# Optimization experiments

Measured on AMD Instinct MI355X. Metric: run time of the kernel, lower is better.

## Reference

```python
import jax, jax.numpy as jnp
import numpy as np

P, C, D = 65536, 64, 256

def setup_inputs() -> dict:
    key = jax.random.key(0)
    k1, k2, k3, k4 = jax.random.split(key, 4)
    return {
        "protos1": jax.random.normal(k1, (P, D), dtype=jnp.float32),
        "protos2": jax.random.normal(k2, (P, D), dtype=jnp.float32),
        "W": jax.random.normal(k3, (D, D), dtype=jnp.float32) / np.float32(np.sqrt(D)),
        "b": jax.random.normal(k4, (D,), dtype=jnp.float32),
        "num_classes": C,
    }

def _pairwise_dist(x, y):
    # x: (C, n, D), y: (C, m, D) -> squared-euclidean-style dists (C, n, m)
    xs = jnp.sum(x * x, axis=-1)[:, :, None]
    ys = jnp.sum(y * y, axis=-1)[:, None, :]
    return xs + ys - 2.0 * jnp.einsum('cid,cjd->cij', x, y)

def reference(protos1, protos2, W, b, num_classes):
    nc = int(num_classes)
    d = protos1.shape[-1]
    # prototypes[c::num_classes] for all c at once: (P,D) -> (P//C, C, D) -> (C, P//C, D)
    p1 = protos1.reshape(-1, nc, d).transpose(1, 0, 2)
    p2 = protos2.reshape(-1, nc, d).transpose(1, 0, 2)
    # transition: nn.Linear -> x @ W.T + b ; inverse: (x - b) @ inv(W.T)
    p2_inv = (p2 - b) @ jnp.linalg.inv(W.T)
    p1_fwd = p1 @ W.T + b
    a = _pairwise_dist(p1, p2_inv)          # (C, n, n)
    bb = _pairwise_dist(p2, p1_fwd)         # (C, n, n)
    proto_losses_source = jnp.mean(jnp.min(a, axis=2), axis=1)   # (C,)
    proto_losses_target = jnp.mean(jnp.min(bb, axis=2), axis=1)  # (C,)
    return jnp.stack([proto_losses_source, proto_losses_target])  # (2, C)
```

## Files before the change

### kernel.cpp

```cpp
#include <hip/hip_runtime.h>

#define D 256
#define NC 64

using u16 = unsigned short;
using u32 = unsigned int;

typedef __attribute__((ext_vector_type(8))) short bfv8;
typedef __attribute__((ext_vector_type(4))) float f32x4;
typedef __attribute__((ext_vector_type(2))) int v2i;

__device__ __forceinline__ float bf2f(u32 u) {
  union { u32 i; float f; } v; v.i = u << 16; return v.f;
}
__device__ __forceinline__ u16 f2bf(float f) {
  union { float f; u32 i; } v; v.f = f;
  u32 x = v.i;
  return (u16)((x + 0x7FFFu + ((x >> 16) & 1u)) >> 16);
}
__device__ __forceinline__ u32 pk2(float a, float b) {
  return (u32)f2bf(a) | ((u32)f2bf(b) << 16);
}
__device__ __forceinline__ size_t cmrow(int g) {
  return (size_t)(((g & 63) << 10) | (g >> 6));
}

__device__ __forceinline__ void gload_lds16(const void* src, void* dst) {
  __builtin_amdgcn_global_load_lds(
      (const __attribute__((address_space(1))) void*)src,
      (__attribute__((address_space(3))) void*)dst, 16, 0, 0);
}

#define K1_LDS 74240
#define DISTP_LDS 70144

__device__ void gj_body(const float* __restrict__ W, float* __restrict__ IW,
                        char* smem) {
  float (*Ml)[20]    = (float(*)[20])smem;
  float (*Arow)[256] = (float(*)[256])(smem + 20480);
  float (*G)[256]    = (float(*)[256])(smem + 36864);
  u16*  Gfrag        = (u16*)(smem + 53248);
  float (*Pinv)[20]  = (float(*)[20])(smem + 69888);
  const int t = threadIdx.x, w = t >> 6, l = t & 63;
  const int lj = l & 15, lh = l >> 4;
  const int r0 = 16 * w;
  const bool lo32 = (l < 32);

  f32x4 x[16];
#pragma unroll
  for (int ct = 0; ct < 16; ++ct)
#pragma unroll
    for (int reg = 0; reg < 4; ++reg)
      x[ct][reg] = W[(size_t)(r0 + 4 * lh + reg) * D + 16 * ct + lj];

  for (int s = 0; s < 16; ++s) {
#pragma unroll
    for (int ct = 0; ct < 16; ++ct)
      if (ct == s)
#pragma unroll
        for (int reg = 0; reg < 4; ++reg)
          Ml[r0 + 4 * lh + reg][lj] = x[ct][reg];
    if (w == s) {
#pragma unroll
      for (int ct = 0; ct < 16; ++ct)
#pragma unroll
        for (int reg = 0; reg < 4; ++reg)
          Arow[4 * lh + reg][16 * ct + lj] = x[ct][reg];
    }
    bfv8 afr;
    {
      const int row = r0 + lj;
      float4 f0 = *(const float4*)&Ml[row][8 * (lh & 1)];
      float4 f1 = *(const float4*)&Ml[row][8 * (lh & 1) + 4];
      const float fv[8] = {f0.x, f0.y, f0.z, f0.w, f1.x, f1.y, f1.z, f1.w};
      union { bfv8 v; u16 e[8]; } A;
      if (lh < 2) {
#pragma unroll
        for (int e = 0; e < 8; ++e) A.e[e] = f2bf(-fv[e]);
      } else {
#pragma unroll
        for (int e = 0; e < 8; ++e) {
          const float hi = bf2f(f2bf(fv[e]));
          A.e[e] = f2bf(-(fv[e] - hi));
        }
      }
      afr = A.v;
    }
    __syncthreads();
    if (t < 16) {
      float p[16];
      {
        float4 rr0 = *(const float4*)&Ml[16 * s + t][0];
        float4 rr1 = *(const float4*)&Ml[16 * s + t][4];
        float4 rr2 = *(const float4*)&Ml[16 * s + t][8];
        float4 rr3 = *(const float4*)&Ml[16 * s + t][12];
        p[0] = rr0.x; p[1] = rr0.y; p[2] = rr0.z; p[3] = rr0.w;
        p[4] = rr1.x; p[5] = rr1.y; p[6] = rr1.z; p[7] = rr1.w;
        p[8] = rr2.x; p[9] = rr2.y; p[10] = rr2.z; p[11] = rr2.w;
        p[12] = rr3.x; p[13] = rr3.y; p[14] = rr3.z; p[15] = rr3.w;
      }
#pragma unroll
      for (int pp = 0; pp < 16; ++pp) {
        float u[16];
#pragma unroll
        for (int j = 0; j < 16; ++j)
          u[j] = __int_as_float(__builtin_amdgcn_readlane(__float_as_int(p[j]), pp));
        const float pv = u[pp];
        const float d = 1.0f / pv;
        if (t == pp) {
#pragma unroll
          for (int j = 0; j < 16; ++j) p[j] = u[j] * d;
          p[pp] = d;
        } else {
          const float md = p[pp] * d;
          u[pp] = pv + 1.0f;
#pragma unroll
          for (int j = 0; j < 16; ++j) p[j] = fmaf(-md, u[j], p[j]);
        }
      }
#pragma unroll
      for (int j = 0; j < 16; ++j) Pinv[t][j] = p[j];
    }
    __syncthreads();
    {
      const bool inC = ((l >> 2) == s);
      const int co = (l & 3) << 2;
      const int gct = l >> 2;
      const int kk = w;
      float4 g = make_float4(0.f, 0.f, 0.f, 0.f);
#pragma unroll
      for (int q = 0; q < 16; ++q) {
        const float pv = Pinv[kk][q];
        const float4 av = *(const float4*)&Arow[q][4 * l];
        g.x = fmaf(pv, av.x, g.x); g.y = fmaf(pv, av.y, g.y);
        g.z = fmaf(pv, av.z, g.z); g.w = fmaf(pv, av.w, g.w);
      }
      if (inC) {
        g.x = Pinv[kk][co + 0] + (kk == co + 0 ? 1.f : 0.f);
        g.y = Pinv[kk][co + 1] + (kk == co + 1 ? 1.f : 0.f);
        g.z = Pinv[kk][co + 2] + (kk == co + 2 ? 1.f : 0.f);
        g.w = Pinv[kk][co + 3] + (kk == co + 3 ? 1.f : 0.f);
      }
      *(float4*)&G[kk][4 * l] = g;
      const int e0 = kk & 7;
      const int lbase = 16 * (kk >> 3);
      const float gv[4] = {g.x, g.y, g.z, g.w};
#pragma unroll
      for (int cc = 0; cc < 4; ++cc) {
        const int cl = 4 * (l & 3) + cc;
        const u16 hi = f2bf(gv[cc]);
        const u16 lo = f2bf(gv[cc] - bf2f(hi));
        Gfrag[gct * 520 + (lbase + cl) * 8 + e0] = hi;
        Gfrag[gct * 520 + (32 + lbase + cl) * 8 + e0] = lo;
      }
    }
    __syncthreads();
    if (w != s) {
#pragma unroll
      for (int ct = 0; ct < 16; ++ct) {
        union { bfv8 v; uint4 u; } B1, B2;
        B1.v = *(const bfv8*)&Gfrag[ct * 520 + l * 8];
#if __has_builtin(__builtin_amdgcn_permlane32_swap)
        {
          v2i r;
          r = __builtin_amdgcn_permlane32_swap((int)B1.u.x, (int)B1.u.x, false, false);
          B2.u.x = lo32 ? (u32)r.y : (u32)r.x;
          r = __builtin_amdgcn_permlane32_swap((int)B1.u.y, (int)B1.u.y, false, false);
          B2.u.y = lo32 ? (u32)r.y : (u32)r.x;
          r = __builtin_amdgcn_permlane32_swap((int)B1.u.z, (int)B1.u.z, false, false);
          B2.u.z = lo32 ? (u32)r.y : (u32)r.x;
          r = __builtin_amdgcn_permlane32_swap((int)B1.u.w, (int)B1.u.w, false, false);
          B2.u.w = lo32 ? (u32)r.y : (u32)r.x;
        }
#else
        B2.v = *(const bfv8*)&Gfrag[ct * 520 + (l ^ 32) * 8];
#endif
        x[ct] = __builtin_amdgcn_mfma_f32_16x16x32_bf16(afr, B1.v, x[ct], 0, 0, 0);
        x[ct] = __builtin_amdgcn_mfma_f32_16x16x32_bf16(afr, B2.v, x[ct], 0, 0, 0);
      }
    } else {
#pragma unroll
      for (int ct = 0; ct < 16; ++ct) {
        if (ct == s) {
#pragma unroll
          for (int reg = 0; reg < 4; ++reg)
            x[ct][reg] = Pinv[4 * lh + reg][lj];
        } else {
#pragma unroll
          for (int reg = 0; reg < 4; ++reg)
            x[ct][reg] = G[4 * lh + reg][16 * ct + lj];
        }
      }
    }
    __syncthreads();
  }
#pragma unroll
  for (int ct = 0; ct < 16; ++ct)
#pragma unroll
    for (int reg = 0; reg < 4; ++reg)
      IW[(size_t)(r0 + 4 * lh + reg) * D + 16 * ct + lj] = x[ct][reg];
}

__device__ void convnorm_role(const float* __restrict__ P, u16* __restrict__ Pb,
                              float* __restrict__ nrm, int blk) {
  const int tx = threadIdx.x;
  const int r = tx >> 2, q = tx & 3;
  const int g = blk * 256 + r;
  const float* src = P + (size_t)g * D + q * 64;
  u16* dst = Pb + cmrow(g) * D + q * 64;
  float ss = 0.f;
#pragma unroll
  for (int g4 = 0; g4 < 8; ++g4) {
    float4 v0 = *(const float4*)(src + g4 * 8);
    float4 v1 = *(const float4*)(src + g4 * 8 + 4);
    ss = fmaf(v0.x, v0.x, fmaf(v0.y, v0.y, fmaf(v0.z, v0.z, fmaf(v0.w, v0.w, ss))));
    ss = fmaf(v1.x, v1.x, fmaf(v1.y, v1.y, fmaf(v1.z, v1.z, fmaf(v1.w, v1.w, ss))));
    uint4 w4;
    w4.x = pk2(v0.x, v0.y); w4.y = pk2(v0.z, v0.w);
    w4.z = pk2(v1.x, v1.y); w4.w = pk2(v1.z, v1.w);
    *(uint4*)(dst + g4 * 8) = w4;
  }
  ss += __shfl_xor(ss, 1, 64);
  ss += __shfl_xor(ss, 2, 64);
  if (q == 0) nrm[cmrow(g)] = ss;
}

template <int MODE>
__device__ void distp_body(const float* __restrict__ Pj,
                           const float* __restrict__ Wf,
                           const u16* __restrict__ BrowsBF,
                           const float* __restrict__ biasv,
                           const float* __restrict__ PanF,
                           const u16* __restrict__ PanBF,
                           const float* __restrict__ nB,
                           float* __restrict__ pmind, int bid, char* smem) {
  const int lb = (bid & 7) * 64 + (bid >> 3);
  const int c = lb >> 3, jt = lb & 7;
  const int tx = threadIdx.x, ww = tx >> 6, l = tx & 63;
  const int mw = ww >> 3, nw = ww & 7, l4 = l >> 4, lm = l & 15;
  char* Ab = smem;
  float* nfpart = (float*)(smem + 65536);
  float* minbuf = (float*)(smem + 65536);
  float* nAb = (float*)(smem + 69632);
  float* nbpart = (float*)(smem + 70144);

  auto issue_chunk = [&](int buf, int ch) {
#pragma unroll
    for (int u = 0; u < 2; ++u) {
      const int chunk = ww * 2 + u, ks = chunk >> 2, n = chunk & 3;
      const u16* src = PanBF + ((size_t)(c << 10) + ch * 64 + n * 16 + lm) * D
                       + ks * 32 + l4 * 8;
      gload_lds16(src, Ab + buf * 32768 + chunk * 1024);
    }
  };
  auto stage_f32 = [&](int buf, int ch) {
#pragma unroll
    for (int u = 0; u < 2; ++u) {
      const int chunk = ww * 2 + u, ks = chunk >> 2, n = chunk & 3;
      const int m = ch * 64 + n * 16 + lm;
      const float* src = PanF + ((size_t)m * 64 + c) * D + ks * 32 + l4 * 8;
      float4 v0 = *(const float4*)src;
      float4 v1 = *(const float4*)(src + 4);
      uint4 w4;
      w4.x = pk2(v0.x, v0.y); w4.y = pk2(v0.z, v0.w);
      w4.z = pk2(v1.x, v1.y); w4.w = pk2(v1.z, v1.w);
      *(uint4*)(Ab + buf * 32768 + chunk * 1024 + l * 16) = w4;
      float ss = fmaf(v0.x, v0.x, fmaf(v0.y, v0.y, fmaf(v0.z, v0.z, v0.w * v0.w)));
      ss = fmaf(v1.x, v1.x, fmaf(v1.y, v1.y, fmaf(v1.z, v1.z, fmaf(v1.w, v1.w, ss))));
      ss += __shfl_xor(ss, 16, 64);
      ss += __shfl_xor(ss, 32, 64);
      if (l4 == 0) nbpart[buf * 512 + ks * 64 + n * 16 + lm] = ss;
    }
  };

  bfv8 bfr[2][8];
  if (MODE == 0) {
#pragma unroll
    for (int nf2 = 0; nf2 < 2; ++nf2)
#pragma unroll
      for (int ks = 0; ks < 8; ++ks) {
        const float* wsrc = Wf + (size_t)(nw * 32 + nf2 * 16 + lm) * D + ks * 32 + l4 * 8;
        float4 b0 = *(const float4*)wsrc;
        float4 b1 = *(const float4*)(wsrc + 4);
        union { bfv8 v; uint4 u; } cv;
        cv.u.x = pk2(b0.x, b0.y); cv.u.y = pk2(b0.z, b0.w);
        cv.u.z = pk2(b1.x, b1.y); cv.u.w = pk2(b1.z, b1.w);
        bfr[nf2][ks] = cv.v;
      }
  } else {
#pragma unroll
    for (int nf2 = 0; nf2 < 2; ++nf2)
#pragma unroll
      for (int ks = 0; ks < 8; ++ks)
        bfr[nf2][ks] = *(const bfv8*)(BrowsBF +
            (size_t)(nw * 32 + nf2 * 16 + lm) * D + ks * 32 + l4 * 8);
  }
  {
    const int r = tx >> 3, sg = tx & 7;
    const float* arow = Pj + ((size_t)(jt * 128 + r) * NC + c) * D + sg * 32;
#pragma unroll
    for (int g2 = 0; g2 < 4; ++g2) {
      float4 v0 = *(const float4*)(arow + g2 * 8);
      float4 v1 = *(const float4*)(arow + g2 * 8 + 4);
      uint4 w4;
      w4.x = pk2(v0.x, v0.y); w4.y = pk2(v0.z, v0.w);
      w4.z = pk2(v1.x, v1.y); w4.w = pk2(v1.z, v1.w);
      *(uint4*)(Ab + (sg * 8 + (r >> 4)) * 1024 + ((r & 15) + g2 * 16) * 16) = w4;
    }
  }
  __syncthreads();
  const bfv8* A8 = (const bfv8*)Ab;
  f32x4 acc[4][2];
#pragma unroll
  for (int mf = 0; mf < 4; ++mf) {
    acc[mf][0] = f32x4{0.f, 0.f, 0.f, 0.f};
    acc[mf][1] = f32x4{0.f, 0.f, 0.f, 0.f};
  }
#pragma unroll
  for (int ks = 0; ks < 8; ++ks)
#pragma unroll
    for (int mf = 0; mf < 4; ++mf) {
      bfv8 a = A8[(ks * 8 + mw * 4 + mf) * 64 + l];
      acc[mf][0] = __builtin_amdgcn_mfma_f32_16x16x32_bf16(a, bfr[0][ks], acc[mf][0], 0, 0, 0);
      acc[mf][1] = __builtin_amdgcn_mfma_f32_16x16x32_bf16(a, bfr[1][ks], acc[mf][1], 0, 0, 0);
    }
  float bias[2];
  if (MODE == 0) {
#pragma unroll
    for (int nf2 = 0; nf2 < 2; ++nf2)
      bias[nf2] = biasv[nw * 32 + nf2 * 16 + lm];
  } else {
#pragma unroll
    for (int nf2 = 0; nf2 < 2; ++nf2) {
      float pd = 0.f;
#pragma unroll
      for (int ks = 0; ks < 8; ++ks) {
        float4 b0 = *(const float4*)(biasv + ks * 32 + l4 * 8);
        float4 b1 = *(const float4*)(biasv + ks * 32 + l4 * 8 + 4);
        pd = fmaf(b0.x, bf2f((u16)bfr[nf2][ks][0]), pd);
        pd = fmaf(b0.y, bf2f((u16)bfr[nf2][ks][1]), pd);
        pd = fmaf(b0.z, bf2f((u16)bfr[nf2][ks][2]), pd);
        pd = fmaf(b0.w, bf2f((u16)bfr[nf2][ks][3]), pd);
        pd = fmaf(b1.x, bf2f((u16)bfr[nf2][ks][4]), pd);
        pd = fmaf(b1.y, bf2f((u16)bfr[nf2][ks][5]), pd);
        pd = fmaf(b1.z, bf2f((u16)bfr[nf2][ks][6]), pd);
        pd = fmaf(b1.w, bf2f((u16)bfr[nf2][ks][7]), pd);
      }
      pd += __shfl_xor(pd, 16, 64);
      pd += __shfl_xor(pd, 32, 64);
      bias[nf2] = -pd;
    }
  }
  __syncthreads();
  u16* tile = (u16*)Ab;
#pragma unroll
  for (int mf = 0; mf < 4; ++mf)
#pragma unroll
    for (int rr = 0; rr < 4; ++rr) {
      const int j = mw * 64 + mf * 16 + l4 * 4 + rr;
      float v2 = 0.f;
#pragma unroll
      for (int nf2 = 0; nf2 < 2; ++nf2) {
        const float v = acc[mf][nf2][rr] + bias[nf2];
        const u16 hv = f2bf(v);
        tile[(((nw * 8 + mw * 4 + mf) << 6) + ((nf2 * 2 + (lm >> 3)) << 4)
              + l4 * 4 + rr) * 8 + (lm & 7)] = hv;
        const float vr = bf2f(hv);
        v2 = fmaf(vr, vr, v2);
      }
      v2 += __shfl_xor(v2, 1, 64);
      v2 += __shfl_xor(v2, 2, 64);
      v2 += __shfl_xor(v2, 4, 64);
      v2 += __shfl_xor(v2, 8, 64);
      if (lm == 0) nfpart[nw * 128 + j] = v2;
    }
  __syncthreads();
  const int jw = ww >> 2, iw = ww & 3;
  bfv8 afr[2][8];
#pragma unroll
  for (int jj = 0; jj < 2; ++jj)
#pragma unroll
    for (int ks = 0; ks < 8; ++ks)
      afr[jj][ks] = A8[(ks * 8 + jw * 2 + jj) * 64 + l];
  __syncthreads();
  if (MODE == 0) stage_f32(0, 0); else issue_chunk(0, 0);
  if (tx < 128) {
    float s = 0.f;
#pragma unroll
    for (int q = 0; q < 8; ++q) s += nfpart[q * 128 + tx];
    nAb[tx] = s;
  }
  __syncthreads();
  float naj[2][4];
#pragma unroll
  for (int jj = 0; jj < 2; ++jj)
#pragma unroll
    for (int rr = 0; rr < 4; ++rr)
      naj[jj][rr] = nAb[jw * 32 + jj * 16 + l4 * 4 + rr];
  const float* nBc = (MODE == 1) ? nB + (c << 10) : nullptr;
  const size_t obase = (size_t)(c * 8 + jt) * 1024;
  for (int ch = 0; ch < 16; ++ch) {
    if (ch < 15) {
      if (MODE == 0) stage_f32((ch + 1) & 1, ch + 1);
      else issue_chunk((ch + 1) & 1, ch + 1);
    }
    const bfv8* B8 = (const bfv8*)(Ab + (ch & 1) * 32768);
    f32x4 a2[2];
    a2[0] = f32x4{0.f, 0.f, 0.f, 0.f};
    a2[1] = f32x4{0.f, 0.f, 0.f, 0.f};
#pragma unroll
    for (int ks = 0; ks < 8; ++ks) {
      bfv8 b = B8[(ks * 4 + iw) * 64 + l];
      a2[0] = __builtin_amdgcn_mfma_f32_16x16x32_bf16(afr[0][ks], b, a2[0], 0, 0, 0);
      a2[1] = __builtin_amdgcn_mfma_f32_16x16x32_bf16(afr[1][ks], b, a2[1], 0, 0, 0);
    }
    float nb;
    if (MODE == 0) {
      const float* nbp = nbpart + (ch & 1) * 512;
      nb = nbp[iw * 16 + lm];
#pragma unroll
      for (int ks = 1; ks < 8; ++ks) nb += nbp[ks * 64 + iw * 16 + lm];
    } else {
      nb = nBc[ch * 64 + iw * 16 + lm];
    }
    float mm = 3.0e38f;
#pragma unroll
    for (int jj = 0; jj < 2; ++jj)
#pragma unroll
      for (int rr = 0; rr < 4; ++rr) {
        const float dd = nb + naj[jj][rr] - 2.0f * a2[jj][rr];
        mm = fminf(mm, dd);
      }
    mm = fminf(mm, __shfl_xor(mm, 16, 64));
    mm = fminf(mm, __shfl_xor(mm, 32, 64));
    if (l4 == 0) minbuf[jw * 64 + iw * 16 + lm] = mm;
    __syncthreads();
    if (tx < 64) {
      float m = minbuf[tx];
#pragma unroll
      for (int q = 1; q < 4; ++q) m = fminf(m, minbuf[q * 64 + tx]);
      pmind[obase + ch * 64 + tx] = m;
    }
    __syncthreads();
  }
}

__global__ __launch_bounds__(1024, 1) void k1_kernel(
    const float* __restrict__ p1, const float* __restrict__ p2,
    const float* __restrict__ W, const float* __restrict__ bv,
    float* __restrict__ pmin1, float* __restrict__ IWa,
    u16* __restrict__ p1b, float* __restrict__ n1) {
  extern __shared__ char smem[];
  const int b = blockIdx.x;
  if (b == 0) {
    gj_body(W, IWa, smem);
  } else if (b <= 512) {
    distp_body<0>(p1, W, nullptr, bv, p2, nullptr, nullptr, pmin1, b - 1, smem);
  } else {
    convnorm_role(p1, p1b, n1, b - 513);
  }
}

__global__ __launch_bounds__(256) void ns_fused(const float* __restrict__ W,
                                                const float* __restrict__ X,
                                                u16* __restrict__ Yb) {
  __shared__ float Xc[256][8];
  __shared__ float Rc[256][8];
  const int jc = blockIdx.x * 8, t = threadIdx.x;
  {
    float4 xa = *(const float4*)&X[(size_t)t * D + jc];
    float4 xb = *(const float4*)&X[(size_t)t * D + jc + 4];
    Xc[t][0] = xa.x; Xc[t][1] = xa.y; Xc[t][2] = xa.z; Xc[t][3] = xa.w;
    Xc[t][4] = xb.x; Xc[t][5] = xb.y; Xc[t][6] = xb.z; Xc[t][7] = xb.w;
  }
  __syncthreads();
  float r[8] = {0.f, 0.f, 0.f, 0.f, 0.f, 0.f, 0.f, 0.f};
#pragma unroll 4
  for (int k = 0; k < D; ++k) {
    const float wv = W[(size_t)t * D + k];
#pragma unroll
    for (int q = 0; q < 8; ++q) r[q] = fmaf(wv, Xc[k][q], r[q]);
  }
#pragma unroll
  for (int q = 0; q < 8; ++q)
    Rc[t][q] = ((t - jc) == q ? 2.0f : 0.0f) - r[q];
  __syncthreads();
  float y[8] = {0.f, 0.f, 0.f, 0.f, 0.f, 0.f, 0.f, 0.f};
#pragma unroll 4
  for (int k = 0; k < D; ++k) {
    const float xv = X[(size_t)t * D + k];
#pragma unroll
    for (int q = 0; q < 8; ++q) y[q] = fmaf(xv, Rc[k][q], y[q]);
  }
#pragma unroll
  for (int q = 0; q < 8; ++q)
    Yb[(size_t)t * D + jc + q] = f2bf(y[q]);
}

__global__ __launch_bounds__(1024, 1) void k3_kernel(
    const float* __restrict__ p2, const u16* __restrict__ IWb,
    const float* __restrict__ bv, const u16* __restrict__ p1b,
    const float* __restrict__ n1, float* __restrict__ pmin0) {
  extern __shared__ char smem[];
  distp_body<1>(p2, nullptr, IWb, bv, nullptr, p1b, n1, pmin0, blockIdx.x, smem);
}

__global__ __launch_bounds__(256) void final_kernel(const float* __restrict__ pmin,
                                                    float* __restrict__ out) {
  __shared__ float ws4[4];
  const int dc = blockIdx.x, tx = threadIdx.x;
  const float* base = pmin + (size_t)dc * 8192;
  float s = 0.f;
#pragma unroll
  for (int t = 0; t < 4; ++t) {
    const int i = t * 256 + tx;
    float m = base[i];
#pragma unroll
    for (int j = 1; j < 8; ++j) m = fminf(m, base[j * 1024 + i]);
    s += m;
  }
#pragma unroll
  for (int off = 32; off; off >>= 1) s += __shfl_xor(s, off, 64);
  if ((tx & 63) == 0) ws4[tx >> 6] = s;
  __syncthreads();
  if (tx == 0)
    out[dc] = (ws4[0] + ws4[1] + ws4[2] + ws4[3]) * (1.0f / 1024.0f);
}

extern "C" void kernel_launch(void* const* d_in, const int* in_sizes, int n_in,
                              void* d_out, int out_size, void* d_ws, size_t ws_size,
                              hipStream_t stream) {
  const float* p1 = (const float*)d_in[0];
  const float* p2 = (const float*)d_in[1];
  const float* W  = (const float*)d_in[2];
  const float* bv = (const float*)d_in[3];
  float* out = (float*)d_out;
  char* ws = (char*)d_ws;
  float* n1  = (float*)(ws);
  float* IWa = (float*)(ws + (256 << 10));
  u16* IWb   = (u16*)(ws + (512 << 10));
  float* pmin = (float*)(ws + (1 << 20));
  u16* p1b   = (u16*)(ws + (6u << 20));
  float* pmin0 = pmin;
  float* pmin1 = pmin + 524288;

  hipFuncSetAttribute((const void*)k1_kernel,
                      hipFuncAttributeMaxDynamicSharedMemorySize, K1_LDS);
  hipFuncSetAttribute((const void*)k3_kernel,
                      hipFuncAttributeMaxDynamicSharedMemorySize, DISTP_LDS);

  k1_kernel<<<769, 1024, K1_LDS, stream>>>(p1, p2, W, bv, pmin1, IWa, p1b, n1);
  ns_fused<<<32, 256, 0, stream>>>(W, IWa, IWb);
  k3_kernel<<<512, 1024, DISTP_LDS, stream>>>(p2, IWb, bv, p1b, n1, pmin0);
  final_kernel<<<128, 256, 0, stream>>>(pmin, out);
}
```

Measured before the change: 328.8 us.

## Pre-convert protos2 to bf16 with norms in a separate kernel before distance pass

Adds a k0 kernel that converts protos2 to class-major bf16 and computes its row norms up front. The MODE 0 distance pass can then stream B tiles straight into LDS with global_load_lds, as MODE 1 already does, instead of doing strided fp32 loads, in-register conversion and per-chunk norm reductions. This drops the nbpart LDS buffer and shrinks K1's LDS. The cost is an extra launch plus a write and reread of a 32 MB bf16 copy, and the conversion can no longer overlap with k1's other roles.

```diff
diff --git a/kernel.cpp b/kernel.cpp
--- a/kernel.cpp
+++ b/kernel.cpp
@@ -31,7 +31,7 @@
       (__attribute__((address_space(3))) void*)dst, 16, 0, 0);
 }
 
-#define K1_LDS 74240
+#define K1_LDS 71168
 #define DISTP_LDS 70144
 
 __device__ void gj_body(const float* __restrict__ W, float* __restrict__ IW,
@@ -230,7 +230,6 @@
                            const float* __restrict__ Wf,
                            const u16* __restrict__ BrowsBF,
                            const float* __restrict__ biasv,
-                           const float* __restrict__ PanF,
                            const u16* __restrict__ PanBF,
                            const float* __restrict__ nB,
                            float* __restrict__ pmind, int bid, char* smem) {
@@ -242,7 +241,6 @@
   float* nfpart = (float*)(smem + 65536);
   float* minbuf = (float*)(smem + 65536);
   float* nAb = (float*)(smem + 69632);
-  float* nbpart = (float*)(smem + 70144);
 
   auto issue_chunk = [&](int buf, int ch) {
 #pragma unroll
@@ -251,25 +249,6 @@
       const u16* src = PanBF + ((size_t)(c << 10) + ch * 64 + n * 16 + lm) * D
                        + ks * 32 + l4 * 8;
       gload_lds16(src, Ab + buf * 32768 + chunk * 1024);
-    }
-  };
-  auto stage_f32 = [&](int buf, int ch) {
-#pragma unroll
-    for (int u = 0; u < 2; ++u) {
-      const int chunk = ww * 2 + u, ks = chunk >> 2, n = chunk & 3;
-      const int m = ch * 64 + n * 16 + lm;
-      const float* src = PanF + ((size_t)m * 64 + c) * D + ks * 32 + l4 * 8;
-      float4 v0 = *(const float4*)src;
-      float4 v1 = *(const float4*)(src + 4);
-      uint4 w4;
-      w4.x = pk2(v0.x, v0.y); w4.y = pk2(v0.z, v0.w);
-      w4.z = pk2(v1.x, v1.y); w4.w = pk2(v1.z, v1.w);
-      *(uint4*)(Ab + buf * 32768 + chunk * 1024 + l * 16) = w4;
-      float ss = fmaf(v0.x, v0.x, fmaf(v0.y, v0.y, fmaf(v0.z, v0.z, v0.w * v0.w)));
-      ss = fmaf(v1.x, v1.x, fmaf(v1.y, v1.y, fmaf(v1.z, v1.z, fmaf(v1.w, v1.w, ss))));
-      ss += __shfl_xor(ss, 16, 64);
-      ss += __shfl_xor(ss, 32, 64);
-      if (l4 == 0) nbpart[buf * 512 + ks * 64 + n * 16 + lm] = ss;
     }
   };
 
@@ -383,7 +362,7 @@
     for (int ks = 0; ks < 8; ++ks)
       afr[jj][ks] = A8[(ks * 8 + jw * 2 + jj) * 64 + l];
   __syncthreads();
-  if (MODE == 0) stage_f32(0, 0); else issue_chunk(0, 0);
+  issue_chunk(0, 0);
   if (tx < 128) {
     float s = 0.f;
 #pragma unroll
@@ -397,13 +376,10 @@
 #pragma unroll
     for (int rr = 0; rr < 4; ++rr)
       naj[jj][rr] = nAb[jw * 32 + jj * 16 + l4 * 4 + rr];
-  const float* nBc = (MODE == 1) ? nB + (c << 10) : nullptr;
+  const float* nBc = nB + (c << 10);
   const size_t obase = (size_t)(c * 8 + jt) * 1024;
   for (int ch = 0; ch < 16; ++ch) {
-    if (ch < 15) {
-      if (MODE == 0) stage_f32((ch + 1) & 1, ch + 1);
-      else issue_chunk((ch + 1) & 1, ch + 1);
-    }
+    if (ch < 15) issue_chunk((ch + 1) & 1, ch + 1);
     const bfv8* B8 = (const bfv8*)(Ab + (ch & 1) * 32768);
     f32x4 a2[2];
     a2[0] = f32x4{0.f, 0.f, 0.f, 0.f};
@@ -414,15 +390,7 @@
       a2[0] = __builtin_amdgcn_mfma_f32_16x16x32_bf16(afr[0][ks], b, a2[0], 0, 0, 0);
       a2[1] = __builtin_amdgcn_mfma_f32_16x16x32_bf16(afr[1][ks], b, a2[1], 0, 0, 0);
     }
-    float nb;
-    if (MODE == 0) {
-      const float* nbp = nbpart + (ch & 1) * 512;
-      nb = nbp[iw * 16 + lm];
-#pragma unroll
-      for (int ks = 1; ks < 8; ++ks) nb += nbp[ks * 64 + iw * 16 + lm];
-    } else {
-      nb = nBc[ch * 64 + iw * 16 + lm];
-    }
+    const float nb = nBc[ch * 64 + iw * 16 + lm];
     float mm = 3.0e38f;
 #pragma unroll
     for (int jj = 0; jj < 2; ++jj)
@@ -445,17 +413,23 @@
   }
 }
 
+__global__ __launch_bounds__(1024, 1) void k0_kernel(
+    const float* __restrict__ p2, u16* __restrict__ p2b,
+    float* __restrict__ n2) {
+  convnorm_role(p2, p2b, n2, blockIdx.x);
+}
+
 __global__ __launch_bounds__(1024, 1) void k1_kernel(
-    const float* __restrict__ p1, const float* __restrict__ p2,
-    const float* __restrict__ W, const float* __restrict__ bv,
-    float* __restrict__ pmin1, float* __restrict__ IWa,
-    u16* __restrict__ p1b, float* __restrict__ n1) {
+    const float* __restrict__ p1, const float* __restrict__ W,
+    const float* __restrict__ bv, const u16* __restrict__ p2b,
+    const float* __restrict__ n2, float* __restrict__ pmin1,
+    float* __restrict__ IWa, u16* __restrict__ p1b, float* __restrict__ n1) {
   extern __shared__ char smem[];
   const int b = blockIdx.x;
   if (b == 0) {
     gj_body(W, IWa, smem);
   } else if (b <= 512) {
-    distp_body<0>(p1, W, nullptr, bv, p2, nullptr, nullptr, pmin1, b - 1, smem);
+    distp_body<0>(p1, W, nullptr, bv, p2b, n2, pmin1, b - 1, smem);
   } else {
     convnorm_role(p1, p1b, n1, b - 513);
   }
@@ -502,7 +476,7 @@
     const float* __restrict__ bv, const u16* __restrict__ p1b,
     const float* __restrict__ n1, float* __restrict__ pmin0) {
   extern __shared__ char smem[];
-  distp_body<1>(p2, nullptr, IWb, bv, nullptr, p1b, n1, pmin0, blockIdx.x, smem);
+  distp_body<1>(p2, nullptr, IWb, bv, p1b, n1, pmin0, blockIdx.x, smem);
 }
 
 __global__ __launch_bounds__(256) void final_kernel(const float* __restrict__ pmin,
@@ -537,10 +511,12 @@
   float* out = (float*)d_out;
   char* ws = (char*)d_ws;
   float* n1  = (float*)(ws);
-  float* IWa = (float*)(ws + (256 << 10));
-  u16* IWb   = (u16*)(ws + (512 << 10));
+  float* n2  = (float*)(ws + (256 << 10));
+  float* IWa = (float*)(ws + (512 << 10));
+  u16* IWb   = (u16*)(ws + (768 << 10));
   float* pmin = (float*)(ws + (1 << 20));
   u16* p1b   = (u16*)(ws + (6u << 20));
+  u16* p2b   = (u16*)(ws + (38u << 20));
   float* pmin0 = pmin;
   float* pmin1 = pmin + 524288;
 
@@ -549,7 +525,9 @@
   hipFuncSetAttribute((const void*)k3_kernel,
                       hipFuncAttributeMaxDynamicSharedMemorySize, DISTP_LDS);
 
-  k1_kernel<<<769, 1024, K1_LDS, stream>>>(p1, p2, W, bv, pmin1, IWa, p1b, n1);
+  k0_kernel<<<256, 1024, 0, stream>>>(p2, p2b, n2);
+  k1_kernel<<<769, 1024, K1_LDS, stream>>>(p1, W, bv, p2b, n2,
+                                           pmin1, IWa, p1b, n1);
   ns_fused<<<32, 256, 0, stream>>>(W, IWa, IWb);
   k3_kernel<<<512, 1024, DISTP_LDS, stream>>>(p2, IWb, bv, p1b, n1, pmin0);
   final_kernel<<<128, 256, 0, stream>>>(pmin, out);
```

Result: faster. 299.5 us (-8.9%).
